# Optimization experiments

Measured on AMD Instinct MI355X. Metric: run time of the kernel, lower is better.

Reference implementation:

```python
import jax, jax.numpy as jnp
import numpy as np

C = 64
CQ = C // 8
CR = C // 16  # SE reduction


def _conv1x1(x, W, b):
    # x: [B,C,V,T], W: [O,C], b: [O]
    return jnp.einsum('bcvt,oc->bovt', x, W) + b[None, :, None, None]


def setup_inputs() -> dict:
    key = jax.random.key(0)
    ks = jax.random.split(key, 10)
    B, V, T = 4, 224, 224
    s = 0.05
    return {
        'x': jax.random.normal(ks[0], (B, C, V, T), jnp.float32),
        'Wq': jax.random.normal(ks[1], (CQ, C), jnp.float32) * s,
        'bq': jax.random.normal(ks[2], (CQ,), jnp.float32) * s,
        'Wk': jax.random.normal(ks[3], (CQ, C), jnp.float32) * s,
        'bk': jax.random.normal(ks[4], (CQ,), jnp.float32) * s,
        'Wv': jax.random.normal(ks[5], (C, C), jnp.float32) * s,
        'bv': jax.random.normal(ks[6], (C,), jnp.float32) * s,
        'gamma': jax.random.normal(ks[7], (), jnp.float32) * 0.5,
        'W1': jax.random.normal(ks[8], (CR, C), jnp.float32) * s,
        'W2': jax.random.normal(ks[9], (C, CR), jnp.float32) * s,
    }


def reference(x, Wq, bq, Wk, bk, Wv, bv, gamma, W1, W2):
    B, Cc, V, T = x.shape
    # ---- CrissCrossAttention (add_input=True) ----
    q = _conv1x1(x, Wq, bq)  # [B,CQ,V,T]
    k = _conv1x1(x, Wk, bk)  # [B,CQ,V,T]
    v = _conv1x1(x, Wv, bv)  # [B,C,V,T]
    # column (H) attention: energy_H[b,v,t,u] = q[b,:,v,t].k[b,:,u,t], diag -inf
    energy_H = jnp.einsum('bcvt,bcut->bvtu', q, k)
    diag = jnp.eye(V, dtype=bool)[:, None, :]  # [V,1,V]
    energy_H = jnp.where(diag[None], -jnp.inf, energy_H)
    # row (W) attention: energy_W[b,v,t,s] = q[b,:,v,t].k[b,:,v,s]
    energy_W = jnp.einsum('bcvt,bcvs->bvts', q, k)
    concate = jax.nn.softmax(jnp.concatenate([energy_H, energy_W], axis=-1), axis=-1)
    att_H = concate[..., :V]       # [B,V,T,V]
    att_W = concate[..., V:V + T]  # [B,V,T,T]
    out_H = jnp.einsum('bcut,bvtu->bcvt', v, att_H)
    out_W = jnp.einsum('bcvs,bvts->bcvt', v, att_W)
    x1 = gamma * (out_H + out_W) + x
    # ---- SELayer (mul_input=True) ----
    y = jnp.mean(x, axis=(2, 3))                # [B,C]
    y = jax.nn.relu(jnp.einsum('bc,rc->br', y, W1))
    y = jax.nn.sigmoid(jnp.einsum('br,cr->bc', y, W2))
    x2 = x * y[:, :, None, None]
    # ---- structure == 'parallel' ----
    return x1 + x2
```

## Files before the change

### kernel.cpp

```cpp
#include <hip/hip_runtime.h>
#include <math.h>

#define CC 64
#define CQv 8
#define CRv 4
#define BB 4
#define RR 224
#define TT 224
#define NN (RR*TT)
#define LOG2E 1.4426950408889634f

typedef __attribute__((ext_vector_type(8))) short short8;
typedef __attribute__((ext_vector_type(4))) float f32x4;

__device__ __forceinline__ f32x4 mfma_bf16(short8 a, short8 b, f32x4 c){
    return __builtin_amdgcn_mfma_f32_16x16x32_bf16(a, b, c, 0, 0, 0);
}

__device__ __forceinline__ ushort f2bf(float f){
    union { float f; unsigned u; } v; v.f = f;
    unsigned r = v.u + 0x7fffu + ((v.u >> 16) & 1u);
    return (ushort)(r >> 16);
}
__device__ __forceinline__ float bf2f(ushort u){
    return __uint_as_float((unsigned)u << 16);
}
__device__ __forceinline__ unsigned packbf(float a, float b){
    return __builtin_amdgcn_perm(__float_as_uint(b), __float_as_uint(a), 0x07060302u);
}
__device__ __forceinline__ int vswz(int row, int uslot){
    return (uslot ^ (row & 7) ^ ((row >> 3) & 7)) << 4;
}

__global__ __launch_bounds__(256) void k_qkv(
    const float* __restrict__ x,
    const float* __restrict__ Wq, const float* __restrict__ bq,
    const float* __restrict__ Wk, const float* __restrict__ bk,
    const float* __restrict__ Wv, const float* __restrict__ bv,
    ushort* __restrict__ qB, ushort* __restrict__ kB, ushort* __restrict__ vB,
    float* __restrict__ partial)
{
    const int tid = threadIdx.x;
    const int w = tid >> 6, l = tid & 63, l15 = l & 15, lg = l >> 4;
    const int blk = blockIdx.x;
    const int b = blk / 196, pb = blk - b*196;
    const int n0 = pb*256;
    const float* xb = x + (size_t)b*CC*NN;

    short8 afr[5][2];
#pragma unroll
    for (int ot = 0; ot < 5; ++ot) {
        int oo = ot*16 + l15;
        const float* wr = (oo < 8) ? (Wq + oo*64)
                        : (oo < 16) ? (Wk + (oo-8)*64)
                                    : (Wv + (oo-16)*64);
        float scl = (oo >= 8 && oo < 16) ? LOG2E : 1.0f;
#pragma unroll
        for (int ks = 0; ks < 2; ++ks) {
            const float* p = wr + ks*32 + lg*8;
            float4 w0 = *(const float4*)p, w1 = *(const float4*)(p+4);
            short8 f;
            f[0]=f2bf(w0.x*scl); f[1]=f2bf(w0.y*scl); f[2]=f2bf(w0.z*scl); f[3]=f2bf(w0.w*scl);
            f[4]=f2bf(w1.x*scl); f[5]=f2bf(w1.y*scl); f[6]=f2bf(w1.z*scl); f[7]=f2bf(w1.w*scl);
            afr[ot][ks] = f;
        }
    }
    f32x4 binit[5];
#pragma unroll
    for (int ot = 0; ot < 5; ++ot) {
        const float* bp;
        float scl = 1.0f;
        if (ot == 0) { bp = (lg < 2) ? (bq + lg*4) : (bk + (lg-2)*4); if (lg >= 2) scl = LOG2E; }
        else           bp = bv + (ot-1)*16 + lg*4;
        float4 bb4 = *(const float4*)bp;
        binit[ot] = (f32x4){bb4.x*scl, bb4.y*scl, bb4.z*scl, bb4.w*scl};
    }

    float msum[16];
#pragma unroll
    for (int i = 0; i < 16; ++i) msum[i] = 0.f;

#pragma unroll
    for (int j = 0; j < 4; ++j) {
        int n = n0 + (w*4 + j)*16 + l15;
        short8 bfr[2];
#pragma unroll
        for (int ks = 0; ks < 2; ++ks) {
            const float* xp = xb + (size_t)(ks*32 + lg*8)*NN + n;
            short8 f;
#pragma unroll
            for (int e = 0; e < 8; ++e) {
                float xv = xp[(size_t)e*NN];
                f[e] = f2bf(xv);
                msum[ks*8 + e] += xv;
            }
            bfr[ks] = f;
        }
#pragma unroll
        for (int ot = 0; ot < 5; ++ot) {
            f32x4 acc = binit[ot];
            acc = mfma_bf16(afr[ot][0], bfr[0], acc);
            acc = mfma_bf16(afr[ot][1], bfr[1], acc);
            ushort4 pk;
            pk.x = f2bf(acc[0]); pk.y = f2bf(acc[1]);
            pk.z = f2bf(acc[2]); pk.w = f2bf(acc[3]);
            if (ot == 0) {
                ushort* dst = (lg < 2) ? (qB + ((size_t)b*NN + n)*8 + lg*4)
                                       : (kB + ((size_t)b*NN + n)*8 + (lg-2)*4);
                *(ushort4*)dst = pk;
            } else {
                int oc = (ot-1)*16 + lg*4;
                *(ushort4*)(vB + ((size_t)b*NN + n)*64 + oc) = pk;
            }
        }
    }

#pragma unroll
    for (int i = 0; i < 16; ++i) {
        float s = msum[i];
        s += __shfl_xor(s, 1); s += __shfl_xor(s, 2);
        s += __shfl_xor(s, 4); s += __shfl_xor(s, 8);
        msum[i] = s;
    }
    __shared__ float msums[4][4][16];
    if (l15 == 0) {
#pragma unroll
        for (int i = 0; i < 16; ++i) msums[w][lg][i] = msum[i];
    }
    __syncthreads();
    if (tid < 64) {
        int c = tid;
        int lgi = (c >> 3) & 3, ii = (c >> 5)*8 + (c & 7);
        float t = msums[0][lgi][ii] + msums[1][lgi][ii] + msums[2][lgi][ii] + msums[3][lgi][ii];
        partial[(size_t)blk*64 + c] = t;
    }
}

__global__ __launch_bounds__(256) void k_tq(const uint4* __restrict__ qs, const uint4* __restrict__ ks,
                                            uint4* __restrict__ qd, uint4* __restrict__ kd)
{
    __shared__ uint4 tile[32][33];
    int z = blockIdx.z;
    int b = z & 3;
    const uint4* sp = ((z >= 4) ? ks : qs) + (size_t)b*NN;
    uint4*       dp = ((z >= 4) ? kd : qd) + (size_t)b*NN;
    int t0 = blockIdx.x*32, r0 = blockIdx.y*32;
    int tx = threadIdx.x & 31, ty = threadIdx.x >> 5;
#pragma unroll
    for (int j = 0; j < 4; ++j) { int lr = ty + 8*j; tile[lr][tx] = sp[(size_t)(r0+lr)*224 + t0 + tx]; }
    __syncthreads();
#pragma unroll
    for (int j = 0; j < 4; ++j) { int lt = ty + 8*j; dp[(size_t)(t0+lt)*224 + r0 + tx] = tile[tx][lt]; }
}

__global__ __launch_bounds__(256, 3) void k_pv(const ushort* __restrict__ qA, const ushort* __restrict__ kA,
                                               const ushort* __restrict__ qB, const ushort* __restrict__ kB,
                                               const ushort* __restrict__ vB,
                                               ushort* __restrict__ outA, ushort* __restrict__ outB,
                                               float* __restrict__ ZHt, float* __restrict__ ZWt)
{
    __shared__ __align__(16) ushort Vt[64*256];
    __shared__ __align__(16) ushort Kh[224*8];

    const int tid = threadIdx.x;
    const int bid = blockIdx.x;
    const bool HM = bid < BB*224;
    const int blk = HM ? bid : bid - BB*224;
    const int b = blk / 224, o = blk - b*224;
    const ushort* Qsrc = (HM ? qA : qB) + (size_t)blk*1792;
    const ushort* Ksrc = (HM ? kA : kB) + (size_t)blk*1792;
    ushort* op = (HM ? outA : outB) + (size_t)blk*14336;
    float*  Zt = (HM ? ZHt : ZWt) + (size_t)blk*224;

    {
        const uint4* vbase = (const uint4*)vB;
        for (int gi = tid; gi < 448; gi += 256) {
            int ublk = gi >> 3, sub = gi & 7;
            int u0 = ublk << 2;
            size_t base, stride;
            if (HM) { base = ((size_t)b*NN + (size_t)u0*224 + o)*8 + sub; stride = 1792; }
            else    { base = ((size_t)blk*224 + u0)*8 + sub;              stride = 8;    }
            uint4 r0 = vbase[base], r1 = vbase[base+stride], r2 = vbase[base+2*stride], r3 = vbase[base+3*stride];
            const ushort* p0 = (const ushort*)&r0;
            const ushort* p1 = (const ushort*)&r1;
            const ushort* p2 = (const ushort*)&r2;
            const ushort* p3 = (const ushort*)&r3;
            int half = (ublk & 1) * 8;
#pragma unroll
            for (int j = 0; j < 8; ++j) {
                int c = sub*8 + j;
                ushort4 col; col.x = p0[j]; col.y = p1[j]; col.z = p2[j]; col.w = p3[j];
                *(ushort4*)((char*)Vt + c*512 + vswz(c, ublk >> 1) + half) = col;
            }
        }
    }
    if (tid < 224) ((uint4*)Kh)[tid] = ((const uint4*)Ksrc)[tid];
    __syncthreads();

    const int w = tid >> 6, l = tid & 63;
    const int l15 = l & 15, lg = l >> 4;
    const short8 zfr = {0,0,0,0,0,0,0,0};
    const f32x4 zacc = {0.f,0.f,0.f,0.f};

    const int src0 = (l15 + ((lg & 1) << 5)) << 2;
    const int src1 = src0 + 64;
    const bool hi = (lg >= 2);

    for (int ch = w; ch < 14; ch += 4) {
        short8 qf = zfr;
        if (lg == 0) qf = *(const short8*)(Qsrc + (size_t)(ch*16 + l15)*8);
        f32x4 acc0 = zacc, acc1 = zacc, acc2 = zacc, acc3 = zacc;
        float zsum = 0.f;
#pragma unroll 1
        for (int ks = 0; ks < 7; ++ks) {
            short8 kf0 = *(const short8*)(Kh + (size_t)(ks*32 + l15)*8);
            short8 kf1 = *(const short8*)(Kh + (size_t)(ks*32 + 16 + l15)*8);
            f32x4 e0 = mfma_bf16(kf0, qf, zacc);
            f32x4 e1 = mfma_bf16(kf1, qf, zacc);
            float a0[4], a1[4];
#pragma unroll
            for (int g = 0; g < 4; ++g) {
                a0[g] = __builtin_amdgcn_exp2f(e0[g]);
                a1[g] = __builtin_amdgcn_exp2f(e1[g]);
            }
            if (HM && (ch >> 1) == ks) {
                if ((ch & 1) == 0) {
#pragma unroll
                    for (int g = 0; g < 4; ++g) if (lg*4 + g == l15) a0[g] = 0.f;
                } else {
#pragma unroll
                    for (int g = 0; g < 4; ++g) if (lg*4 + g == l15) a1[g] = 0.f;
                }
            }
            zsum += ((a0[0]+a0[1]) + (a0[2]+a0[3])) + ((a1[0]+a1[1]) + (a1[2]+a1[3]));
            unsigned p00 = packbf(a0[0], a0[1]), p01 = packbf(a0[2], a0[3]);
            unsigned p10 = packbf(a1[0], a1[1]), p11 = packbf(a1[2], a1[3]);
            unsigned s0 = hi ? p10 : p00;
            unsigned s1 = hi ? p11 : p01;
            int fx = __builtin_amdgcn_ds_bpermute(src0, (int)s0);
            int fy = __builtin_amdgcn_ds_bpermute(src0, (int)s1);
            int fz = __builtin_amdgcn_ds_bpermute(src1, (int)s0);
            int fw = __builtin_amdgcn_ds_bpermute(src1, (int)s1);
            int4 fi; fi.x = fx; fi.y = fy; fi.z = fz; fi.w = fw;
            short8 af = *(short8*)&fi;
            {
                short8 vf0 = *(const short8*)((const char*)Vt + (size_t)(l15)*512       + vswz(l15,      ks*4 + lg));
                short8 vf1 = *(const short8*)((const char*)Vt + (size_t)(16 + l15)*512  + vswz(16 + l15, ks*4 + lg));
                short8 vf2 = *(const short8*)((const char*)Vt + (size_t)(32 + l15)*512  + vswz(32 + l15, ks*4 + lg));
                short8 vf3 = *(const short8*)((const char*)Vt + (size_t)(48 + l15)*512  + vswz(48 + l15, ks*4 + lg));
                acc0 = mfma_bf16(vf0, af, acc0);
                acc1 = mfma_bf16(vf1, af, acc1);
                acc2 = mfma_bf16(vf2, af, acc2);
                acc3 = mfma_bf16(vf3, af, acc3);
            }
        }
        zsum += __shfl_xor(zsum, 16);
        zsum += __shfl_xor(zsum, 32);
        if (lg == 0) Zt[ch*16 + l15] = zsum;
        {
            int pos = ch*16 + l15;
            f32x4 av[4] = {acc0, acc1, acc2, acc3};
#pragma unroll
            for (int ct = 0; ct < 4; ++ct) {
                ushort4 pk;
                pk.x = f2bf(av[ct][0]); pk.y = f2bf(av[ct][1]);
                pk.z = f2bf(av[ct][2]); pk.w = f2bf(av[ct][3]);
                *(ushort4*)(op + (size_t)pos*64 + ct*16 + lg*4) = pk;
            }
        }
    }
}

__global__ __launch_bounds__(256) void k_aux(const float* __restrict__ ZHt, const float* __restrict__ ZWt,
                                             const float* __restrict__ gammap,
                                             const float* __restrict__ partial,
                                             const float* __restrict__ W1, const float* __restrict__ W2,
                                             float* __restrict__ Zi, float* __restrict__ y2)
{
    const int blk = blockIdx.x;
    if (blk < 196) {
        __shared__ float tile[32][33];
        int b = blk / 49, rem = blk - b*49;
        int t0 = (rem % 7)*32, v0 = (rem / 7)*32;
        int tx = threadIdx.x & 31, ty = threadIdx.x >> 5;
        float g = gammap[0];
#pragma unroll
        for (int j = 0; j < 4; ++j) {
            int tl = ty + 8*j;
            tile[tl][tx] = ZHt[((size_t)(b*224 + t0 + tl))*224 + v0 + tx];
        }
        __syncthreads();
#pragma unroll
        for (int j = 0; j < 4; ++j) {
            int vl = ty + 8*j;
            size_t i = ((size_t)(b*224 + v0 + vl))*224 + t0 + tx;
            float zs = tile[tx][vl] + ZWt[i];
            Zi[i] = g * __builtin_amdgcn_rcpf(zs);
        }
    } else {
        __shared__ float mean_s[4][64];
        int tid = threadIdx.x;
        int b = tid >> 6, c = tid & 63;
        float s = 0.f;
        for (int i = 0; i < 196; ++i) s += partial[((size_t)(b*196 + i))*64 + c];
        mean_s[b][c] = s * (1.0f/NN);
        __syncthreads();
        float h[CRv];
#pragma unroll
        for (int j = 0; j < CRv; ++j) {
            float t = 0.f;
#pragma unroll
            for (int cc = 0; cc < CC; ++cc) t += W1[j*CC + cc] * mean_s[b][cc];
            h[j] = fmaxf(t, 0.f);
        }
        float s2 = 0.f;
#pragma unroll
        for (int j = 0; j < CRv; ++j) s2 += W2[c*CRv + j] * h[j];
        y2[tid] = 1.f/(1.f + __expf(-s2));
    }
}

__global__ __launch_bounds__(256) void k_final(const float* __restrict__ x,
                                               const ushort* __restrict__ outA,
                                               const ushort* __restrict__ outB,
                                               const float* __restrict__ Zi,
                                               const float* __restrict__ y2,
                                               float* __restrict__ out)
{
    __shared__ float Ls[2][16][65];
    __shared__ float sc[64];
    const int b = blockIdx.z;
    const int v0 = blockIdx.y*16, t0 = blockIdx.x*16;
    const int tid = threadIdx.x;
    if (tid < 64) sc[tid] = 1.f + y2[b*64 + tid];

    const int tl = tid >> 4, cg = tid & 15;
    const int tg = tid & 3, cw = tid >> 2;

    const ushort* pA = outA + (size_t)b*NN*64;
    const ushort* pB = outB + (size_t)b*NN*64;
    __syncthreads();

    for (int vl = 0; vl < 16; ++vl) {
        const int v = v0 + vl;
        const int buf = vl & 1;
        {
            const ushort* a4 = pA + ((size_t)(t0 + tl)*224 + v)*64 + cg*4;
            const ushort* b4 = pB + ((size_t)v*224 + (t0 + tl))*64 + cg*4;
            uint2 ra = *(const uint2*)a4;
            uint2 rb = *(const uint2*)b4;
            const ushort* qa = (const ushort*)&ra;
            const ushort* qb = (const ushort*)&rb;
            float zi = Zi[(size_t)b*NN + (size_t)v*224 + t0 + tl];
#pragma unroll
            for (int j = 0; j < 4; ++j)
                Ls[buf][tl][cg*4 + j] = (bf2f(qa[j]) + bf2f(qb[j])) * zi;
        }
        __syncthreads();
        {
            float s = sc[cw];
            size_t idx = (size_t)(b*64 + cw)*NN + (size_t)v*224 + t0 + tg*4;
            float4 xv = *(const float4*)(x + idx);
            float4 o;
            o.x = xv.x*s + Ls[buf][tg*4+0][cw];
            o.y = xv.y*s + Ls[buf][tg*4+1][cw];
            o.z = xv.z*s + Ls[buf][tg*4+2][cw];
            o.w = xv.w*s + Ls[buf][tg*4+3][cw];
            *(float4*)(out + idx) = o;
        }
    }
}

extern "C" void kernel_launch(void* const* d_in, const int* in_sizes, int n_in,
                              void* d_out, int out_size, void* d_ws, size_t ws_size,
                              hipStream_t stream)
{
    const float* x  = (const float*)d_in[0];
    const float* Wq = (const float*)d_in[1];
    const float* bq = (const float*)d_in[2];
    const float* Wk = (const float*)d_in[3];
    const float* bk = (const float*)d_in[4];
    const float* Wv = (const float*)d_in[5];
    const float* bv = (const float*)d_in[6];
    const float* gm = (const float*)d_in[7];
    const float* W1 = (const float*)d_in[8];
    const float* W2 = (const float*)d_in[9];
    float* out = (float*)d_out;

    constexpr size_t QSZ = (size_t)BB*NN*CQv;
    constexpr size_t VSZ = (size_t)BB*NN*CC;
    constexpr size_t SSZ = (size_t)BB*NN;

    ushort* qB = (ushort*)d_ws;
    ushort* kB = qB + QSZ;
    ushort* vB = kB + QSZ;
    ushort* qA = vB + VSZ;
    ushort* kA = qA + QSZ;
    ushort* outA = kA + QSZ;
    ushort* outB = outA + VSZ;
    float*  ZHt = (float*)(outB + VSZ);
    float*  ZWt = ZHt + SSZ;
    float*  Zi  = ZWt + SSZ;
    float*  partial = Zi + SSZ;
    float*  y2 = partial + (size_t)BB*196*64;
    (void)ws_size; (void)in_sizes; (void)n_in; (void)out_size;

    k_qkv<<<BB*196, 256, 0, stream>>>(x, Wq, bq, Wk, bk, Wv, bv, qB, kB, vB, partial);
    k_tq<<<dim3(7,7,8), 256, 0, stream>>>((const uint4*)qB, (const uint4*)kB, (uint4*)qA, (uint4*)kA);

    k_pv<<<2*BB*224, 256, 0, stream>>>(qA, kA, qB, kB, vB, outA, outB, ZHt, ZWt);
    k_aux<<<197, 256, 0, stream>>>(ZHt, ZWt, gm, partial, W1, W2, Zi, y2);

    k_final<<<dim3(14,14,BB), 256, 0, stream>>>(x, outA, outB, Zi, y2, out);
}
```

Measured before the change: 114.9 us.

## Remove bpermute by re-laying V in LDS and process two query chunks per pass

Changes the LDS layout of the transposed V tile so the exp-probability fragments produced by the energy MFMA can be fed straight into the PV MFMA, removing the four ds_bpermute shuffles per step. Each wave also handles two query chunks together, sharing K and V fragment loads across eight accumulators to raise MFMA density. The cost is higher register pressure and some wasted MFMA work on the zero-padded second chunk when it is out of range.

```diff
diff --git a/kernel.cpp b/kernel.cpp
--- a/kernel.cpp
+++ b/kernel.cpp
@@ -185,12 +185,15 @@
             const ushort* p1 = (const ushort*)&r1;
             const ushort* p2 = (const ushort*)&r2;
             const ushort* p3 = (const ushort*)&r3;
-            int half = (ublk & 1) * 8;
+            int ks   = ublk >> 3;
+            int th   = (ublk >> 2) & 1;
+            int quad = ublk & 3;
+            int half = th * 8;
 #pragma unroll
             for (int j = 0; j < 8; ++j) {
                 int c = sub*8 + j;
                 ushort4 col; col.x = p0[j]; col.y = p1[j]; col.z = p2[j]; col.w = p3[j];
-                *(ushort4*)((char*)Vt + c*512 + vswz(c, ublk >> 1) + half) = col;
+                *(ushort4*)((char*)Vt + c*512 + vswz(c, ks*4 + quad) + half) = col;
             }
         }
     }
@@ -202,64 +205,99 @@
     const short8 zfr = {0,0,0,0,0,0,0,0};
     const f32x4 zacc = {0.f,0.f,0.f,0.f};
 
-    const int src0 = (l15 + ((lg & 1) << 5)) << 2;
-    const int src1 = src0 + 64;
-    const bool hi = (lg >= 2);
-
-    for (int ch = w; ch < 14; ch += 4) {
-        short8 qf = zfr;
-        if (lg == 0) qf = *(const short8*)(Qsrc + (size_t)(ch*16 + l15)*8);
-        f32x4 acc0 = zacc, acc1 = zacc, acc2 = zacc, acc3 = zacc;
-        float zsum = 0.f;
+#pragma unroll 1
+    for (int p = 0; p < 2; ++p) {
+        const int ch0 = w + p*8;
+        const int ch1 = ch0 + 4;
+        const bool do1 = (ch1 < 14);
+        short8 qf0 = zfr, qf1 = zfr;
+        if (lg == 0) {
+            qf0 = *(const short8*)(Qsrc + (size_t)(ch0*16 + l15)*8);
+            if (do1) qf1 = *(const short8*)(Qsrc + (size_t)(ch1*16 + l15)*8);
+        }
+        f32x4 acc00 = zacc, acc01 = zacc, acc02 = zacc, acc03 = zacc;
+        f32x4 acc10 = zacc, acc11 = zacc, acc12 = zacc, acc13 = zacc;
+        float zs0 = 0.f, zs1 = 0.f;
 #pragma unroll 1
         for (int ks = 0; ks < 7; ++ks) {
             short8 kf0 = *(const short8*)(Kh + (size_t)(ks*32 + l15)*8);
             short8 kf1 = *(const short8*)(Kh + (size_t)(ks*32 + 16 + l15)*8);
-            f32x4 e0 = mfma_bf16(kf0, qf, zacc);
-            f32x4 e1 = mfma_bf16(kf1, qf, zacc);
-            float a0[4], a1[4];
+            f32x4 e00 = mfma_bf16(kf0, qf0, zacc);
+            f32x4 e01 = mfma_bf16(kf1, qf0, zacc);
+            f32x4 e10 = mfma_bf16(kf0, qf1, zacc);
+            f32x4 e11 = mfma_bf16(kf1, qf1, zacc);
+            float a00[4], a01[4], a10[4], a11[4];
 #pragma unroll
             for (int g = 0; g < 4; ++g) {
-                a0[g] = __builtin_amdgcn_exp2f(e0[g]);
-                a1[g] = __builtin_amdgcn_exp2f(e1[g]);
-            }
-            if (HM && (ch >> 1) == ks) {
-                if ((ch & 1) == 0) {
-#pragma unroll
-                    for (int g = 0; g < 4; ++g) if (lg*4 + g == l15) a0[g] = 0.f;
+                a00[g] = __builtin_amdgcn_exp2f(e00[g]);
+                a01[g] = __builtin_amdgcn_exp2f(e01[g]);
+                a10[g] = __builtin_amdgcn_exp2f(e10[g]);
+                a11[g] = __builtin_amdgcn_exp2f(e11[g]);
+            }
+            if (HM && (ch0 >> 1) == ks) {
+                if ((ch0 & 1) == 0) {
+#pragma unroll
+                    for (int g = 0; g < 4; ++g) if (lg*4 + g == l15) a00[g] = 0.f;
                 } else {
 #pragma unroll
-                    for (int g = 0; g < 4; ++g) if (lg*4 + g == l15) a1[g] = 0.f;
+                    for (int g = 0; g < 4; ++g) if (lg*4 + g == l15) a01[g] = 0.f;
                 }
             }
-            zsum += ((a0[0]+a0[1]) + (a0[2]+a0[3])) + ((a1[0]+a1[1]) + (a1[2]+a1[3]));
-            unsigned p00 = packbf(a0[0], a0[1]), p01 = packbf(a0[2], a0[3]);
-            unsigned p10 = packbf(a1[0], a1[1]), p11 = packbf(a1[2], a1[3]);
-            unsigned s0 = hi ? p10 : p00;
-            unsigned s1 = hi ? p11 : p01;
-            int fx = __builtin_amdgcn_ds_bpermute(src0, (int)s0);
-            int fy = __builtin_amdgcn_ds_bpermute(src0, (int)s1);
-            int fz = __builtin_amdgcn_ds_bpermute(src1, (int)s0);
-            int fw = __builtin_amdgcn_ds_bpermute(src1, (int)s1);
-            int4 fi; fi.x = fx; fi.y = fy; fi.z = fz; fi.w = fw;
-            short8 af = *(short8*)&fi;
+            if (HM && do1 && (ch1 >> 1) == ks) {
+                if ((ch1 & 1) == 0) {
+#pragma unroll
+                    for (int g = 0; g < 4; ++g) if (lg*4 + g == l15) a10[g] = 0.f;
+                } else {
+#pragma unroll
+                    for (int g = 0; g < 4; ++g) if (lg*4 + g == l15) a11[g] = 0.f;
+                }
+            }
+            zs0 += ((a00[0]+a00[1]) + (a00[2]+a00[3])) + ((a01[0]+a01[1]) + (a01[2]+a01[3]));
+            zs1 += ((a10[0]+a10[1]) + (a10[2]+a10[3])) + ((a11[0]+a11[1]) + (a11[2]+a11[3]));
+            int4 i0, i1;
+            i0.x = (int)packbf(a00[0], a00[1]); i0.y = (int)packbf(a00[2], a00[3]);
+            i0.z = (int)packbf(a01[0], a01[1]); i0.w = (int)packbf(a01[2], a01[3]);
+            i1.x = (int)packbf(a10[0], a10[1]); i1.y = (int)packbf(a10[2], a10[3]);
+            i1.z = (int)packbf(a11[0], a11[1]); i1.w = (int)packbf(a11[2], a11[3]);
+            short8 af0 = *(short8*)&i0;
+            short8 af1 = *(short8*)&i1;
             {
                 short8 vf0 = *(const short8*)((const char*)Vt + (size_t)(l15)*512       + vswz(l15,      ks*4 + lg));
                 short8 vf1 = *(const short8*)((const char*)Vt + (size_t)(16 + l15)*512  + vswz(16 + l15, ks*4 + lg));
                 short8 vf2 = *(const short8*)((const char*)Vt + (size_t)(32 + l15)*512  + vswz(32 + l15, ks*4 + lg));
                 short8 vf3 = *(const short8*)((const char*)Vt + (size_t)(48 + l15)*512  + vswz(48 + l15, ks*4 + lg));
-                acc0 = mfma_bf16(vf0, af, acc0);
-                acc1 = mfma_bf16(vf1, af, acc1);
-                acc2 = mfma_bf16(vf2, af, acc2);
-                acc3 = mfma_bf16(vf3, af, acc3);
-            }
-        }
-        zsum += __shfl_xor(zsum, 16);
-        zsum += __shfl_xor(zsum, 32);
-        if (lg == 0) Zt[ch*16 + l15] = zsum;
+                acc00 = mfma_bf16(vf0, af0, acc00);
+                acc10 = mfma_bf16(vf0, af1, acc10);
+                acc01 = mfma_bf16(vf1, af0, acc01);
+                acc11 = mfma_bf16(vf1, af1, acc11);
+                acc02 = mfma_bf16(vf2, af0, acc02);
+                acc12 = mfma_bf16(vf2, af1, acc12);
+                acc03 = mfma_bf16(vf3, af0, acc03);
+                acc13 = mfma_bf16(vf3, af1, acc13);
+            }
+        }
+        zs0 += __shfl_xor(zs0, 16);
+        zs0 += __shfl_xor(zs0, 32);
+        zs1 += __shfl_xor(zs1, 16);
+        zs1 += __shfl_xor(zs1, 32);
+        if (lg == 0) {
+            Zt[ch0*16 + l15] = zs0;
+            if (do1) Zt[ch1*16 + l15] = zs1;
+        }
         {
-            int pos = ch*16 + l15;
-            f32x4 av[4] = {acc0, acc1, acc2, acc3};
+            int pos = ch0*16 + l15;
+            f32x4 av[4] = {acc00, acc01, acc02, acc03};
+#pragma unroll
+            for (int ct = 0; ct < 4; ++ct) {
+                ushort4 pk;
+                pk.x = f2bf(av[ct][0]); pk.y = f2bf(av[ct][1]);
+                pk.z = f2bf(av[ct][2]); pk.w = f2bf(av[ct][3]);
+                *(ushort4*)(op + (size_t)pos*64 + ct*16 + lg*4) = pk;
+            }
+        }
+        if (do1) {
+            int pos = ch1*16 + l15;
+            f32x4 av[4] = {acc10, acc11, acc12, acc13};
 #pragma unroll
             for (int ct = 0; ct < 4; ++ct) {
                 ushort4 pk;
```

Measured after the change: 109.9 us. -4.3%, faster.
